# Kernel optimization log

Measured on AMD Instinct MI355X. Metric: run time of the kernel, lower is better.

The kernel has to match this reference:

```python
import jax, jax.numpy as jnp
import numpy as np

B, N, F_IN, S, F_OUT = 16, 128, 8, 8, 64
KN_HID = 32  # kernel_network=[32]
FC_HID = 32


def setup_inputs() -> dict:
    key = jax.random.key(0)
    ks = jax.random.split(key, 13)
    # sparse-ish binary adjacency (batch mode, dense storage)
    A = (jax.random.uniform(ks[0], (B, N, N)) < 0.1).astype(jnp.float32)
    X = jax.random.normal(ks[1], (B, N, F_IN), jnp.float32)
    E = jax.random.normal(ks[2], (B, N, N, S), jnp.float32)
    sc = 0.1
    return {
        "A": A, "X": X, "E": E,
        # ECCConv edge-kernel network: Dense(32, relu) -> Dense(F_IN*F_OUT, linear)
        "kn_w1": jax.random.normal(ks[3], (S, KN_HID), jnp.float32) * sc,
        "kn_b1": jnp.zeros((KN_HID,), jnp.float32),
        "kn_w2": jax.random.normal(ks[4], (KN_HID, F_IN * F_OUT), jnp.float32) * sc,
        "kn_b2": jnp.zeros((F_IN * F_OUT,), jnp.float32),
        # ECCConv root weight + bias
        "root_w": jax.random.normal(ks[5], (F_IN, F_OUT), jnp.float32) * sc,
        "conv_b": jnp.zeros((F_OUT,), jnp.float32),
        # Dense(32, relu)
        "fc_w": jax.random.normal(ks[6], (F_OUT, FC_HID), jnp.float32) * sc,
        "fc_b": jnp.zeros((FC_HID,), jnp.float32),
        # Dense(1, sigmoid)
        "out_w": jax.random.normal(ks[7], (FC_HID, 1), jnp.float32) * sc,
        "out_b": jnp.zeros((1,), jnp.float32),
    }


def reference(A, X, E, kn_w1, kn_b1, kn_w2, kn_b2, root_w, conv_b,
              fc_w, fc_b, out_w, out_b):
    # --- ECCConv (Spektral, batch mode) ---
    # edge-conditioned kernel network: per edge-pair MLP
    h = jax.nn.relu(E @ kn_w1 + kn_b1)            # [B,N,N,32]
    kernel = h @ kn_w2 + kn_b2                    # [B,N,N,F_in*F_out]
    kernel = kernel.reshape(A.shape[0], A.shape[1], A.shape[2], X.shape[-1], root_w.shape[-1])
    kernel = kernel * A[..., None, None]          # mask by adjacency
    # out[b,n,o] = sum_{i,f} kernel[b,n,i,f,o] * X[b,i,f]
    out = jnp.einsum("bnifo,bif->bno", kernel, X)
    out = out + X @ root_w + conv_b               # root weight + bias
    x = jax.nn.relu(out)                          # [B,N,F_out]
    # --- GlobalAvgPool over nodes ---
    x = x.mean(axis=1)                            # [B,F_out]
    # --- Dense head ---
    x = jax.nn.relu(x @ fc_w + fc_b)              # [B,32]
    return jax.nn.sigmoid(x @ out_w + out_b)      # [B,1]
```

## Files before the change

kernel.cpp:

```cpp
#include <hip/hip_runtime.h>
#include <math.h>

#define B_    16
#define N_    128
#define F_IN_ 8
#define S_    8
#define F_OUT_ 64
#define KN_HID_ 32
#define FC_HID_ 32

#define NODE_OFF  0

__global__ __launch_bounds__(256) void k2_fused(
    const float* __restrict__ A, const float* __restrict__ X,
    const float* __restrict__ E,
    const float* __restrict__ kn_w1, const float* __restrict__ kn_b1,
    const float* __restrict__ kn_w2, const float* __restrict__ kn_b2,
    const float* __restrict__ root_w, const float* __restrict__ conv_b,
    float* __restrict__ ws)
{
    __shared__ float Xlds[N_ * F_IN_];
    __shared__ float Tlds[4][2][264];

    const int t    = threadIdx.x;
    const int lane = t & 63;
    const int wave = t >> 6;
    const int h2   = lane >> 5;
    const int j    = lane & 31;
    const int b    = blockIdx.x >> 4;
    const int bn0  = blockIdx.x * 8 + wave * 2;

    ((float4*)Xlds)[t] = ((const float4*)(X + b * N_ * F_IN_))[t];

    float w1j[S_];
#pragma unroll
    for (int s = 0; s < S_; ++s) w1j[s] = kn_w1[s * KN_HID_ + j];
    const float b1j = kn_b1[j];

    float a0[2], a1[2];
#pragma unroll
    for (int nn = 0; nn < 2; ++nn) {
        const int bn = bn0 + nn;
        a0[nn] = A[(size_t)bn * N_ + lane];
        a1[nn] = A[(size_t)bn * N_ + 64 + lane];
    }
    __syncthreads();

    const float4* __restrict__ Xl4 = (const float4*)Xlds;

#pragma unroll
    for (int nn = 0; nn < 2; ++nn) {
        const int bn = bn0 + nn;
        const unsigned long long mA = __ballot(a0[nn] != 0.f);
        const unsigned long long mB = __ballot(a1[nn] != 0.f);
        const float* __restrict__ Eb = E + (size_t)bn * N_ * S_ + (lane & 7);

        float T[4]  = {0.f, 0.f, 0.f, 0.f};
        float xs[4] = {0.f, 0.f, 0.f, 0.f};

#pragma unroll
        for (int half = 0; half < 2; ++half) {
            unsigned long long m = half ? mB : mA;
            if (!m) continue;
            int i = __builtin_ctzll(m) + half * 64;
            m &= m - 1;
            float ev = Eb[i * S_];
            while (true) {
                int inext = -1; float evnext = 0.f;
                if (m) {
                    inext = __builtin_ctzll(m) + half * 64;
                    m &= m - 1;
                    evnext = Eb[inext * S_];
                }
                float hv = b1j;
#pragma unroll
                for (int s = 0; s < S_; ++s)
                    hv += __shfl(ev, s) * w1j[s];
                hv = hv > 0.f ? hv : 0.f;

                const float4 xf = Xl4[i * 2 + h2];
                T[0] += hv * xf.x;  T[1] += hv * xf.y;
                T[2] += hv * xf.z;  T[3] += hv * xf.w;
                xs[0] += xf.x; xs[1] += xf.y; xs[2] += xf.z; xs[3] += xf.w;

                if (inext < 0) break;
                i = inext; ev = evnext;
            }
        }

        float4* __restrict__ Tl4 = (float4*)Tlds[wave][nn];
        Tl4[j * 2 + h2] = make_float4(T[0], T[1], T[2], T[3]);
        if (j == 0)
            Tl4[64 + h2] = make_float4(xs[0], xs[1], xs[2], xs[3]);
    }

    const int q = lane & 15;
    const int g = lane >> 4;
    const float* __restrict__ T0 = Tlds[wave][0];
    const float* __restrict__ T1 = Tlds[wave][1];
    const float4* __restrict__ W4 = (const float4*)kn_w2;
    const float4* __restrict__ B4 = (const float4*)kn_b2;

    float4 acc0 = make_float4(0.f, 0.f, 0.f, 0.f);
    float4 acc1 = make_float4(0.f, 0.f, 0.f, 0.f);
#pragma unroll 8
    for (int kf = g; kf < 256; kf += 4) {
        const float4 w = W4[kf * 16 + q];
        const float t0 = T0[kf], t1 = T1[kf];
        acc0.x += t0 * w.x; acc0.y += t0 * w.y; acc0.z += t0 * w.z; acc0.w += t0 * w.w;
        acc1.x += t1 * w.x; acc1.y += t1 * w.y; acc1.z += t1 * w.z; acc1.w += t1 * w.w;
    }
#pragma unroll
    for (int f = g; f < F_IN_; f += 4) {
        const float4 w = B4[f * 16 + q];
        const float t0 = T0[256 + f], t1 = T1[256 + f];
        acc0.x += t0 * w.x; acc0.y += t0 * w.y; acc0.z += t0 * w.z; acc0.w += t0 * w.w;
        acc1.x += t1 * w.x; acc1.y += t1 * w.y; acc1.z += t1 * w.z; acc1.w += t1 * w.w;
    }

#pragma unroll
    for (int d = 16; d < 64; d <<= 1) {
        acc0.x += __shfl_xor(acc0.x, d); acc0.y += __shfl_xor(acc0.y, d);
        acc0.z += __shfl_xor(acc0.z, d); acc0.w += __shfl_xor(acc0.w, d);
        acc1.x += __shfl_xor(acc1.x, d); acc1.y += __shfl_xor(acc1.y, d);
        acc1.z += __shfl_xor(acc1.z, d); acc1.w += __shfl_xor(acc1.w, d);
    }

    const float4* __restrict__ R4 = (const float4*)root_w;
    const float4 cb = ((const float4*)conv_b)[q];
#pragma unroll
    for (int nn = 0; nn < 2; ++nn) {
        const int bn = bn0 + nn;
        const int n  = bn & (N_ - 1);
        float4 r = (nn == 0) ? acc0 : acc1;
        r.x += cb.x; r.y += cb.y; r.z += cb.z; r.w += cb.w;
#pragma unroll
        for (int f = 0; f < F_IN_; ++f) {
            const float xv = Xlds[n * F_IN_ + f];
            const float4 rw = R4[f * 16 + q];
            r.x += xv * rw.x; r.y += xv * rw.y; r.z += xv * rw.z; r.w += xv * rw.w;
        }
        r.x = r.x > 0.f ? r.x : 0.f;  r.y = r.y > 0.f ? r.y : 0.f;
        r.z = r.z > 0.f ? r.z : 0.f;  r.w = r.w > 0.f ? r.w : 0.f;
        if (g == 0)
            ((float4*)(ws + NODE_OFF + (size_t)bn * F_OUT_))[q] = r;
    }
}

__global__ __launch_bounds__(256) void k3_head(
    const float* __restrict__ fc_w, const float* __restrict__ fc_b,
    const float* __restrict__ out_w, const float* __restrict__ out_b,
    const float* __restrict__ ws, float* __restrict__ out)
{
    const int b = blockIdx.x;
    const int t = threadIdx.x;
    const int o = t & 63;
    const int g = t >> 6;

    float p = 0.f;
    for (int n = g; n < N_; n += 4)
        p += ws[NODE_OFF + (size_t)(b * N_ + n) * F_OUT_ + o];

    __shared__ float red[4][F_OUT_];
    __shared__ float pm[F_OUT_];
    __shared__ float y[FC_HID_];
    red[g][o] = p;
    __syncthreads();

    if (t < F_OUT_)
        pm[t] = (red[0][t] + red[1][t] + red[2][t] + red[3][t]) * (1.0f / (float)N_);
    __syncthreads();

    if (t < FC_HID_) {
        float v = fc_b[t];
#pragma unroll
        for (int o2 = 0; o2 < F_OUT_; ++o2) v += pm[o2] * fc_w[o2 * FC_HID_ + t];
        y[t] = v > 0.f ? v : 0.f;
    }
    __syncthreads();

    if (t == 0) {
        float z = out_b[0];
#pragma unroll
        for (int qq = 0; qq < FC_HID_; ++qq) z += y[qq] * out_w[qq];
        out[b] = 1.f / (1.f + expf(-z));
    }
}

extern "C" void kernel_launch(void* const* d_in, const int* in_sizes, int n_in,
                              void* d_out, int out_size, void* d_ws, size_t ws_size,
                              hipStream_t stream)
{
    const float* A      = (const float*)d_in[0];
    const float* X      = (const float*)d_in[1];
    const float* E      = (const float*)d_in[2];
    const float* kn_w1  = (const float*)d_in[3];
    const float* kn_b1  = (const float*)d_in[4];
    const float* kn_w2  = (const float*)d_in[5];
    const float* kn_b2  = (const float*)d_in[6];
    const float* root_w = (const float*)d_in[7];
    const float* conv_b = (const float*)d_in[8];
    const float* fc_w   = (const float*)d_in[9];
    const float* fc_b   = (const float*)d_in[10];
    const float* out_w  = (const float*)d_in[11];
    const float* out_b  = (const float*)d_in[12];

    float* ws  = (float*)d_ws;
    float* out = (float*)d_out;

    k2_fused<<<B_ * N_ / 8, 256, 0, stream>>>(A, X, E, kn_w1, kn_b1,
                                              kn_w2, kn_b2, root_w, conv_b, ws);
    k3_head<<<B_, 256, 0, stream>>>(fc_w, fc_b, out_w, out_b, ws, out);
}
```

Measured before the change: 107.8 us.

## Assign one node per wave and deepen edge-load prefetch across both halves

Each wave now handles a single node instead of two, which doubles the grid to 512 blocks for more parallelism and shorter per-wave serial edge loops. The edge iteration merges the low and high adjacency masks into one loop and keeps two E loads in flight, to hide gather latency. In exchange, each kn_w2 row read is reused for only one node instead of two, so weight traffic per node doubles, and the X tile is loaded into LDS twice as often.

```diff
diff --git a/kernel.cpp b/kernel.cpp
--- a/kernel.cpp
+++ b/kernel.cpp
@@ -11,6 +11,13 @@
 
 #define NODE_OFF  0
 
+__device__ __forceinline__ int next_edge(unsigned long long& lo,
+                                         unsigned long long& hi) {
+    if (lo) { int i = __builtin_ctzll(lo); lo &= lo - 1; return i; }
+    if (hi) { int i = __builtin_ctzll(hi) + 64; hi &= hi - 1; return i; }
+    return -1;
+}
+
 __global__ __launch_bounds__(256) void k2_fused(
     const float* __restrict__ A, const float* __restrict__ X,
     const float* __restrict__ E,
@@ -20,15 +27,15 @@
     float* __restrict__ ws)
 {
     __shared__ float Xlds[N_ * F_IN_];
-    __shared__ float Tlds[4][2][264];
+    __shared__ float Tlds[4][264];
 
     const int t    = threadIdx.x;
     const int lane = t & 63;
     const int wave = t >> 6;
     const int h2   = lane >> 5;
     const int j    = lane & 31;
-    const int b    = blockIdx.x >> 4;
-    const int bn0  = blockIdx.x * 8 + wave * 2;
+    const int b    = blockIdx.x >> 5;
+    const int bn   = blockIdx.x * 4 + wave;
 
     ((float4*)Xlds)[t] = ((const float4*)(X + b * N_ * F_IN_))[t];
 
@@ -37,114 +44,89 @@
     for (int s = 0; s < S_; ++s) w1j[s] = kn_w1[s * KN_HID_ + j];
     const float b1j = kn_b1[j];
 
-    float a0[2], a1[2];
-#pragma unroll
-    for (int nn = 0; nn < 2; ++nn) {
-        const int bn = bn0 + nn;
-        a0[nn] = A[(size_t)bn * N_ + lane];
-        a1[nn] = A[(size_t)bn * N_ + 64 + lane];
-    }
+    const float a0 = A[(size_t)bn * N_ + lane];
+    const float a1 = A[(size_t)bn * N_ + 64 + lane];
+    unsigned long long mlo = __ballot(a0 != 0.f);
+    unsigned long long mhi = __ballot(a1 != 0.f);
+
     __syncthreads();
 
     const float4* __restrict__ Xl4 = (const float4*)Xlds;
+    const float* __restrict__ Eb = E + (size_t)bn * N_ * S_ + (lane & 7);
 
+    float T[4]  = {0.f, 0.f, 0.f, 0.f};
+    float xs[4] = {0.f, 0.f, 0.f, 0.f};
+
+    int   i0 = next_edge(mlo, mhi);
+    float e0 = (i0 >= 0) ? Eb[i0 * S_] : 0.f;
+    int   i1 = (i0 >= 0) ? next_edge(mlo, mhi) : -1;
+    float e1 = (i1 >= 0) ? Eb[i1 * S_] : 0.f;
+
+    while (i0 >= 0) {
+        const int   i2 = (i1 >= 0) ? next_edge(mlo, mhi) : -1;
+        const float e2 = (i2 >= 0) ? Eb[i2 * S_] : 0.f;
+
+        float hv = b1j;
 #pragma unroll
-    for (int nn = 0; nn < 2; ++nn) {
-        const int bn = bn0 + nn;
-        const unsigned long long mA = __ballot(a0[nn] != 0.f);
-        const unsigned long long mB = __ballot(a1[nn] != 0.f);
-        const float* __restrict__ Eb = E + (size_t)bn * N_ * S_ + (lane & 7);
+        for (int s = 0; s < S_; ++s)
+            hv += __shfl(e0, s) * w1j[s];
+        hv = hv > 0.f ? hv : 0.f;
 
-        float T[4]  = {0.f, 0.f, 0.f, 0.f};
-        float xs[4] = {0.f, 0.f, 0.f, 0.f};
+        const float4 xf = Xl4[i0 * 2 + h2];
+        T[0] += hv * xf.x;  T[1] += hv * xf.y;
+        T[2] += hv * xf.z;  T[3] += hv * xf.w;
+        xs[0] += xf.x; xs[1] += xf.y; xs[2] += xf.z; xs[3] += xf.w;
 
-#pragma unroll
-        for (int half = 0; half < 2; ++half) {
-            unsigned long long m = half ? mB : mA;
-            if (!m) continue;
-            int i = __builtin_ctzll(m) + half * 64;
-            m &= m - 1;
-            float ev = Eb[i * S_];
-            while (true) {
-                int inext = -1; float evnext = 0.f;
-                if (m) {
-                    inext = __builtin_ctzll(m) + half * 64;
-                    m &= m - 1;
-                    evnext = Eb[inext * S_];
-                }
-                float hv = b1j;
-#pragma unroll
-                for (int s = 0; s < S_; ++s)
-                    hv += __shfl(ev, s) * w1j[s];
-                hv = hv > 0.f ? hv : 0.f;
+        i0 = i1; e0 = e1;
+        i1 = i2; e1 = e2;
+    }
 
-                const float4 xf = Xl4[i * 2 + h2];
-                T[0] += hv * xf.x;  T[1] += hv * xf.y;
-                T[2] += hv * xf.z;  T[3] += hv * xf.w;
-                xs[0] += xf.x; xs[1] += xf.y; xs[2] += xf.z; xs[3] += xf.w;
-
-                if (inext < 0) break;
-                i = inext; ev = evnext;
-            }
-        }
-
-        float4* __restrict__ Tl4 = (float4*)Tlds[wave][nn];
-        Tl4[j * 2 + h2] = make_float4(T[0], T[1], T[2], T[3]);
-        if (j == 0)
-            Tl4[64 + h2] = make_float4(xs[0], xs[1], xs[2], xs[3]);
-    }
+    float4* __restrict__ Tl4 = (float4*)Tlds[wave];
+    Tl4[j * 2 + h2] = make_float4(T[0], T[1], T[2], T[3]);
+    if (j == 0)
+        Tl4[64 + h2] = make_float4(xs[0], xs[1], xs[2], xs[3]);
 
     const int q = lane & 15;
     const int g = lane >> 4;
-    const float* __restrict__ T0 = Tlds[wave][0];
-    const float* __restrict__ T1 = Tlds[wave][1];
+    const float* __restrict__ T0 = Tlds[wave];
     const float4* __restrict__ W4 = (const float4*)kn_w2;
     const float4* __restrict__ B4 = (const float4*)kn_b2;
 
-    float4 acc0 = make_float4(0.f, 0.f, 0.f, 0.f);
-    float4 acc1 = make_float4(0.f, 0.f, 0.f, 0.f);
+    float4 acc = make_float4(0.f, 0.f, 0.f, 0.f);
 #pragma unroll 8
     for (int kf = g; kf < 256; kf += 4) {
         const float4 w = W4[kf * 16 + q];
-        const float t0 = T0[kf], t1 = T1[kf];
-        acc0.x += t0 * w.x; acc0.y += t0 * w.y; acc0.z += t0 * w.z; acc0.w += t0 * w.w;
-        acc1.x += t1 * w.x; acc1.y += t1 * w.y; acc1.z += t1 * w.z; acc1.w += t1 * w.w;
+        const float t0 = T0[kf];
+        acc.x += t0 * w.x; acc.y += t0 * w.y; acc.z += t0 * w.z; acc.w += t0 * w.w;
     }
 #pragma unroll
     for (int f = g; f < F_IN_; f += 4) {
         const float4 w = B4[f * 16 + q];
-        const float t0 = T0[256 + f], t1 = T1[256 + f];
-        acc0.x += t0 * w.x; acc0.y += t0 * w.y; acc0.z += t0 * w.z; acc0.w += t0 * w.w;
-        acc1.x += t1 * w.x; acc1.y += t1 * w.y; acc1.z += t1 * w.z; acc1.w += t1 * w.w;
+        const float t0 = T0[256 + f];
+        acc.x += t0 * w.x; acc.y += t0 * w.y; acc.z += t0 * w.z; acc.w += t0 * w.w;
     }
 
 #pragma unroll
     for (int d = 16; d < 64; d <<= 1) {
-        acc0.x += __shfl_xor(acc0.x, d); acc0.y += __shfl_xor(acc0.y, d);
-        acc0.z += __shfl_xor(acc0.z, d); acc0.w += __shfl_xor(acc0.w, d);
-        acc1.x += __shfl_xor(acc1.x, d); acc1.y += __shfl_xor(acc1.y, d);
-        acc1.z += __shfl_xor(acc1.z, d); acc1.w += __shfl_xor(acc1.w, d);
+        acc.x += __shfl_xor(acc.x, d); acc.y += __shfl_xor(acc.y, d);
+        acc.z += __shfl_xor(acc.z, d); acc.w += __shfl_xor(acc.w, d);
     }
 
     const float4* __restrict__ R4 = (const float4*)root_w;
     const float4 cb = ((const float4*)conv_b)[q];
+    const int n = bn & (N_ - 1);
+    float4 r = acc;
+    r.x += cb.x; r.y += cb.y; r.z += cb.z; r.w += cb.w;
 #pragma unroll
-    for (int nn = 0; nn < 2; ++nn) {
-        const int bn = bn0 + nn;
-        const int n  = bn & (N_ - 1);
-        float4 r = (nn == 0) ? acc0 : acc1;
-        r.x += cb.x; r.y += cb.y; r.z += cb.z; r.w += cb.w;
-#pragma unroll
-        for (int f = 0; f < F_IN_; ++f) {
-            const float xv = Xlds[n * F_IN_ + f];
-            const float4 rw = R4[f * 16 + q];
-            r.x += xv * rw.x; r.y += xv * rw.y; r.z += xv * rw.z; r.w += xv * rw.w;
-        }
-        r.x = r.x > 0.f ? r.x : 0.f;  r.y = r.y > 0.f ? r.y : 0.f;
-        r.z = r.z > 0.f ? r.z : 0.f;  r.w = r.w > 0.f ? r.w : 0.f;
-        if (g == 0)
-            ((float4*)(ws + NODE_OFF + (size_t)bn * F_OUT_))[q] = r;
+    for (int f = 0; f < F_IN_; ++f) {
+        const float xv = Xlds[n * F_IN_ + f];
+        const float4 rw = R4[f * 16 + q];
+        r.x += xv * rw.x; r.y += xv * rw.y; r.z += xv * rw.z; r.w += xv * rw.w;
     }
+    r.x = r.x > 0.f ? r.x : 0.f;  r.y = r.y > 0.f ? r.y : 0.f;
+    r.z = r.z > 0.f ? r.z : 0.f;  r.w = r.w > 0.f ? r.w : 0.f;
+    if (g == 0)
+        ((float4*)(ws + NODE_OFF + (size_t)bn * F_OUT_))[q] = r;
 }
 
 __global__ __launch_bounds__(256) void k3_head(
@@ -208,7 +190,7 @@
     float* ws  = (float*)d_ws;
     float* out = (float*)d_out;
 
-    k2_fused<<<B_ * N_ / 8, 256, 0, stream>>>(A, X, E, kn_w1, kn_b1,
+    k2_fused<<<B_ * N_ / 4, 256, 0, stream>>>(A, X, E, kn_w1, kn_b1,
                                               kn_w2, kn_b2, root_w, conv_b, ws);
     k3_head<<<B_, 256, 0, stream>>>(fc_w, fc_b, out_w, out_b, ws, out);
 }
```

Measured after the change: 105.6 us. 1.02x faster.
